# Performance work log

Hardware: AMD Instinct MI355X
Metric: run time of the kernel (lower is better)

Reference implementation:

```python
import jax, jax.numpy as jnp
import numpy as np

N, IN_DIM, OUT_DIM = 2048, 128, 64
ALPHA = 0.2  # LeakyReLU negative slope


def setup_inputs() -> dict:
    key = jax.random.key(0)
    k1, k2, k3 = jax.random.split(key, 3)
    H = jax.random.normal(k1, (N, IN_DIM), dtype=jnp.float32)
    # Xavier-uniform-like init for W [out_dim, in_dim] (torch Linear weight layout)
    limit_w = float(np.sqrt(6.0 / (IN_DIM + OUT_DIM)))
    W = jax.random.uniform(k2, (OUT_DIM, IN_DIM), dtype=jnp.float32,
                           minval=-limit_w, maxval=limit_w)
    limit_a = float(np.sqrt(6.0 / (OUT_DIM + 1)))
    a = jax.random.uniform(k3, (OUT_DIM,), dtype=jnp.float32,
                           minval=-limit_a, maxval=limit_a)
    return {"H": H, "W": W, "a": a}


def reference(H, W, a):
    # Wh: [N, D]
    Wh = H @ W.T
    # e[i, j] = leakyrelu(Wh[i] + Wh[j]) . a   -> [N, N]
    e = jnp.einsum('ijd,d->ij',
                   jax.nn.leaky_relu(Wh[:, None, :] + Wh[None, :, :],
                                     negative_slope=ALPHA),
                   a)
    attention = jax.nn.softmax(e, axis=1)  # softmax over j (columns)
    return attention @ Wh  # [N, D]
```

## Files before the change

kernel.cpp:

```cpp
#include <hip/hip_runtime.h>
#include <hip/hip_fp16.h>

#define N 2048
#define IN_DIM 128
#define D 64
#define ALPHA 0.2f
#define TI 4
#define BLK 512
#define NW (BLK / 64)


typedef _Float16 half2v __attribute__((ext_vector_type(2)));

__device__ __forceinline__ unsigned short f2bf_rne(float f) {
  unsigned int u = __float_as_uint(f);
  unsigned int r = u + 0x7fffu + ((u >> 16) & 1u);
  return (unsigned short)(r >> 16);
}
__device__ __forceinline__ unsigned short f2h_rne(float f) {
  return __half_as_ushort(__float2half(f));
}
#define BF_LO(u) __uint_as_float((u) << 16)
#define BF_HI(u) __uint_as_float((u) & 0xffff0000u)

__device__ __forceinline__ float dot2abs(unsigned s2, unsigned w2,
                                         unsigned a2, float acc) {
  half2v sv = __builtin_bit_cast(half2v, s2);
  half2v wv = __builtin_bit_cast(half2v, w2);
  half2v t = sv + wv;
  unsigned tu = __builtin_bit_cast(unsigned, t) & 0x7fff7fffu;
  return __builtin_amdgcn_fdot2(__builtin_bit_cast(half2v, tu),
                                __builtin_bit_cast(half2v, a2),
                                acc, false);
}

__global__ __launch_bounds__(256) void wh_kernel(
    const float* __restrict__ H, const float* __restrict__ W,
    const float* __restrict__ a, unsigned short* __restrict__ Whb,
    unsigned short* __restrict__ Whh, unsigned int* __restrict__ WhP,
    float* __restrict__ b, unsigned int* __restrict__ ap2) {
  __shared__ float wlds[D][IN_DIM + 1];
  __shared__ float hl[8 * IN_DIM];
  const int t = threadIdx.x;
  const int i0 = blockIdx.x * 8;

  if (blockIdx.x == 0 && t < D / 2) {
    ap2[t] = (unsigned)f2h_rne(0.4f * a[2 * t]) |
             ((unsigned)f2h_rne(0.4f * a[2 * t + 1]) << 16);
  }

  #pragma unroll
  for (int rep = 0; rep < 8; ++rep) {
    int idx = rep * 1024 + t * 4;
    float4 w4 = *(const float4*)&W[idx];
    int d = idx / IN_DIM, k = idx % IN_DIM;
    wlds[d][k] = w4.x; wlds[d][k + 1] = w4.y;
    wlds[d][k + 2] = w4.z; wlds[d][k + 3] = w4.w;
  }
  *(float4*)&hl[t * 4] = *(const float4*)&H[i0 * IN_DIM + t * 4];
  __syncthreads();

  const int wid = t >> 6, lane = t & 63;
  const float av = a[lane];
  #pragma unroll
  for (int r = 0; r < 2; ++r) {
    const int lr = wid * 2 + r;
    const int i = i0 + lr;
    float acc = 0.f;
    #pragma unroll 8
    for (int k = 0; k < IN_DIM; ++k)
      acc = fmaf(hl[lr * IN_DIM + k], wlds[lane][k], acc);
    Whb[i * D + lane] = f2bf_rne(acc);
    unsigned hv = f2h_rne(acc);
    Whh[i * D + lane] = (unsigned short)hv;
    unsigned partner = (unsigned)__shfl_xor((int)hv, 1);
    if (!(lane & 1)) WhP[(lane >> 1) * N + i] = hv | (partner << 16);
    float pb = av * acc;
    #pragma unroll
    for (int off = 32; off; off >>= 1) pb += __shfl_xor(pb, off);
    if (lane == 0) b[i] = 0.6f * pb;
  }
}

__global__ __launch_bounds__(BLK, 4) void attn_kernel(
    const unsigned short* __restrict__ Whb,
    const unsigned short* __restrict__ Whh,
    const unsigned int* __restrict__ WhP,
    const float* __restrict__ b, const unsigned int* __restrict__ ap2,
    float* __restrict__ out) {
  __shared__ float p_lds[TI][N];
  __shared__ float red2s[TI][NW];
  __shared__ float part[NW][TI][D];

  const int t = threadIdx.x;
  const int i0 = blockIdx.x * TI;
  const int wid = t >> 6, lane = t & 63;

  float bs[TI];
  #pragma unroll
  for (int ti = 0; ti < TI; ++ti) bs[ti] = b[i0 + ti];

  const int j0 = t * 4;
  float4 bj = *(const float4*)&b[j0];
  float4 ac[TI];
  #pragma unroll
  for (int ti = 0; ti < TI; ++ti) { ac[ti].x = ac[ti].y = ac[ti].z = ac[ti].w = 0.f; }

  const unsigned int* wp = WhP + j0;
  const uint4* sU = (const uint4*)(Whh + i0 * D);
  const uint4* aU = (const uint4*)ap2;

  uint4 wbuf[2][4], sbuf[2][TI], abuf[2];
  #pragma unroll
  for (int q = 0; q < 4; ++q) wbuf[0][q] = *(const uint4*)&wp[q * N];
  #pragma unroll
  for (int ti = 0; ti < TI; ++ti) sbuf[0][ti] = sU[ti * 8];
  abuf[0] = aU[0];

  #pragma unroll
  for (int c = 0; c < D / 8; ++c) {
    const int cur = c & 1, nxt = cur ^ 1;
    if (c < D / 8 - 1) {
      #pragma unroll
      for (int q = 0; q < 4; ++q)
        wbuf[nxt][q] = *(const uint4*)&wp[((c + 1) * 4 + q) * N];
      #pragma unroll
      for (int ti = 0; ti < TI; ++ti) sbuf[nxt][ti] = sU[ti * 8 + c + 1];
      abuf[nxt] = aU[c + 1];
    }
    #pragma unroll
    for (int q = 0; q < 4; ++q) {
      const unsigned a2 = (q == 0) ? abuf[cur].x : (q == 1) ? abuf[cur].y
                        : (q == 2) ? abuf[cur].z : abuf[cur].w;
      const uint4 w4 = wbuf[cur][q];
      #pragma unroll
      for (int ti = 0; ti < TI; ++ti) {
        const unsigned s2 = (q == 0) ? sbuf[cur][ti].x : (q == 1) ? sbuf[cur][ti].y
                          : (q == 2) ? sbuf[cur][ti].z : sbuf[cur][ti].w;
        ac[ti].x = dot2abs(s2, w4.x, a2, ac[ti].x);
        ac[ti].y = dot2abs(s2, w4.y, a2, ac[ti].y);
        ac[ti].z = dot2abs(s2, w4.z, a2, ac[ti].z);
        ac[ti].w = dot2abs(s2, w4.w, a2, ac[ti].w);
      }
    }
  }

  float s_t[TI];
  #pragma unroll
  for (int ti = 0; ti < TI; ++ti) {
    float4 p4;
    p4.x = __expf(ac[ti].x + bs[ti] + bj.x);
    p4.y = __expf(ac[ti].y + bs[ti] + bj.y);
    p4.z = __expf(ac[ti].z + bs[ti] + bj.z);
    p4.w = __expf(ac[ti].w + bs[ti] + bj.w);
    *(float4*)&p_lds[ti][j0] = p4;
    s_t[ti] = (p4.x + p4.y) + (p4.z + p4.w);
  }
  #pragma unroll
  for (int off = 32; off; off >>= 1) {
    #pragma unroll
    for (int ti = 0; ti < TI; ++ti)
      s_t[ti] += __shfl_xor(s_t[ti], off);
  }
  if (lane == 0) {
    #pragma unroll
    for (int ti = 0; ti < TI; ++ti) red2s[ti][wid] = s_t[ti];
  }
  __syncthreads();

  const int jbase = wid * (N / NW);
  const int hi4 = (lane >> 4) * 4;
  const int col = (lane & 15) * 4;
  float4 acc[TI];
  #pragma unroll
  for (int ti = 0; ti < TI; ++ti) { acc[ti].x = acc[ti].y = acc[ti].z = acc[ti].w = 0.f; }

  uint2 wtile[2][4];
  float4 ptile[2][TI];
  {
    const int r0 = jbase + hi4;
    #pragma unroll
    for (int dd = 0; dd < 4; ++dd)
      wtile[0][dd] = *(const uint2*)&Whb[(r0 + dd) * D + col];
    #pragma unroll
    for (int ti = 0; ti < TI; ++ti)
      ptile[0][ti] = *(const float4*)&p_lds[ti][r0];
  }

  #pragma unroll
  for (int it = 0; it < (N / NW) / 16; ++it) {
    const int cur = it & 1, nxt = cur ^ 1;
    if (it < (N / NW) / 16 - 1) {
      const int r1 = jbase + (it + 1) * 16 + hi4;
      #pragma unroll
      for (int dd = 0; dd < 4; ++dd)
        wtile[nxt][dd] = *(const uint2*)&Whb[(r1 + dd) * D + col];
      #pragma unroll
      for (int ti = 0; ti < TI; ++ti)
        ptile[nxt][ti] = *(const float4*)&p_lds[ti][r1];
    }
    float4 w0, w1, w2, w3;
    w0.x = BF_LO(wtile[cur][0].x); w0.y = BF_HI(wtile[cur][0].x);
    w0.z = BF_LO(wtile[cur][0].y); w0.w = BF_HI(wtile[cur][0].y);
    w1.x = BF_LO(wtile[cur][1].x); w1.y = BF_HI(wtile[cur][1].x);
    w1.z = BF_LO(wtile[cur][1].y); w1.w = BF_HI(wtile[cur][1].y);
    w2.x = BF_LO(wtile[cur][2].x); w2.y = BF_HI(wtile[cur][2].x);
    w2.z = BF_LO(wtile[cur][2].y); w2.w = BF_HI(wtile[cur][2].y);
    w3.x = BF_LO(wtile[cur][3].x); w3.y = BF_HI(wtile[cur][3].x);
    w3.z = BF_LO(wtile[cur][3].y); w3.w = BF_HI(wtile[cur][3].y);
    #pragma unroll
    for (int ti = 0; ti < TI; ++ti) {
      float4 p4 = ptile[cur][ti];
      acc[ti].x = fmaf(p4.x, w0.x, fmaf(p4.y, w1.x, fmaf(p4.z, w2.x, fmaf(p4.w, w3.x, acc[ti].x))));
      acc[ti].y = fmaf(p4.x, w0.y, fmaf(p4.y, w1.y, fmaf(p4.z, w2.y, fmaf(p4.w, w3.y, acc[ti].y))));
      acc[ti].z = fmaf(p4.x, w0.z, fmaf(p4.y, w1.z, fmaf(p4.z, w2.z, fmaf(p4.w, w3.z, acc[ti].z))));
      acc[ti].w = fmaf(p4.x, w0.w, fmaf(p4.y, w1.w, fmaf(p4.z, w2.w, fmaf(p4.w, w3.w, acc[ti].w))));
    }
  }
  #pragma unroll
  for (int ti = 0; ti < TI; ++ti) {
    acc[ti].x += __shfl_xor(acc[ti].x, 16);
    acc[ti].y += __shfl_xor(acc[ti].y, 16);
    acc[ti].z += __shfl_xor(acc[ti].z, 16);
    acc[ti].w += __shfl_xor(acc[ti].w, 16);
    acc[ti].x += __shfl_xor(acc[ti].x, 32);
    acc[ti].y += __shfl_xor(acc[ti].y, 32);
    acc[ti].z += __shfl_xor(acc[ti].z, 32);
    acc[ti].w += __shfl_xor(acc[ti].w, 32);
  }
  if (lane < 16) {
    #pragma unroll
    for (int ti = 0; ti < TI; ++ti)
      *(float4*)&part[wid][ti][lane * 4] = acc[ti];
  }
  __syncthreads();
  if (t < TI * D) {
    const int ti = t >> 6, dd = t & 63;
    float s = 0.f;
    #pragma unroll
    for (int w = 0; w < NW; ++w) s += part[w][ti][dd];
    float4 r0 = *(const float4*)&red2s[ti][0];
    float4 r1 = *(const float4*)&red2s[ti][4];
    float rsum = ((r0.x + r0.y) + (r0.z + r0.w)) +
                 ((r1.x + r1.y) + (r1.z + r1.w));
    out[(i0 + ti) * D + dd] = s * (1.f / rsum);
  }
}

extern "C" void kernel_launch(void* const* d_in, const int* in_sizes, int n_in,
                              void* d_out, int out_size, void* d_ws, size_t ws_size,
                              hipStream_t stream) {
  const float* H = (const float*)d_in[0];
  const float* W = (const float*)d_in[1];
  const float* a = (const float*)d_in[2];
  float* out = (float*)d_out;

  unsigned short* Whb = (unsigned short*)d_ws;
  unsigned short* Whh = Whb + N * D;
  unsigned int* WhP = (unsigned int*)(Whh + N * D);
  float* b = (float*)(WhP + (D / 2) * N);
  unsigned int* ap2 = (unsigned int*)(b + N);

  wh_kernel<<<N / 8, 256, 0, stream>>>(H, W, a, Whb, Whh, WhP, b, ap2);
  attn_kernel<<<N / TI, BLK, 0, stream>>>(Whb, Whh, WhP, b, ap2, out);
}
```

Measured before the change: 33.16 us.

## Use packed fp16 dot2 for attention-weighted sum with pair-interleaved Wh layout

Replaces the bf16 Wh copy with a row-pair interleaved fp16 buffer so the P·Wh accumulation can use packed fp16 dot2 instructions on converted probabilities, halving FMA count and removing bf16 unpacking. The softmax exponent switches to exp2 with a fixed offset and drops the per-row bias term, which cancels in normalisation. wh_kernel now computes two rows per loop sharing the W load. Risks include fp16 overflow or precision loss in probabilities, since the fixed offset does not adapt to row maxima.

```diff
diff --git a/kernel.cpp b/kernel.cpp
--- a/kernel.cpp
+++ b/kernel.cpp
@@ -12,16 +12,9 @@
 
 typedef _Float16 half2v __attribute__((ext_vector_type(2)));
 
-__device__ __forceinline__ unsigned short f2bf_rne(float f) {
-  unsigned int u = __float_as_uint(f);
-  unsigned int r = u + 0x7fffu + ((u >> 16) & 1u);
-  return (unsigned short)(r >> 16);
-}
 __device__ __forceinline__ unsigned short f2h_rne(float f) {
   return __half_as_ushort(__float2half(f));
 }
-#define BF_LO(u) __uint_as_float((u) << 16)
-#define BF_HI(u) __uint_as_float((u) & 0xffff0000u)
 
 __device__ __forceinline__ float dot2abs(unsigned s2, unsigned w2,
                                          unsigned a2, float acc) {
@@ -34,10 +27,19 @@
                                 acc, false);
 }
 
+__device__ __forceinline__ float dot2p(half2v p2, unsigned w2, float acc) {
+  return __builtin_amdgcn_fdot2(p2, __builtin_bit_cast(half2v, w2),
+                                acc, false);
+}
+
+__device__ __forceinline__ half2v cvt_pk(float lo, float hi) {
+  return __builtin_bit_cast(half2v, __builtin_amdgcn_cvt_pkrtz(lo, hi));
+}
+
 __global__ __launch_bounds__(256) void wh_kernel(
     const float* __restrict__ H, const float* __restrict__ W,
-    const float* __restrict__ a, unsigned short* __restrict__ Whb,
-    unsigned short* __restrict__ Whh, unsigned int* __restrict__ WhP,
+    const float* __restrict__ a, unsigned short* __restrict__ Whh,
+    unsigned int* __restrict__ WhP, unsigned int* __restrict__ WhQ,
     float* __restrict__ b, unsigned int* __restrict__ ap2) {
   __shared__ float wlds[D][IN_DIM + 1];
   __shared__ float hl[8 * IN_DIM];
@@ -62,30 +64,41 @@
 
   const int wid = t >> 6, lane = t & 63;
   const float av = a[lane];
-  #pragma unroll
-  for (int r = 0; r < 2; ++r) {
-    const int lr = wid * 2 + r;
-    const int i = i0 + lr;
-    float acc = 0.f;
-    #pragma unroll 8
-    for (int k = 0; k < IN_DIM; ++k)
-      acc = fmaf(hl[lr * IN_DIM + k], wlds[lane][k], acc);
-    Whb[i * D + lane] = f2bf_rne(acc);
-    unsigned hv = f2h_rne(acc);
-    Whh[i * D + lane] = (unsigned short)hv;
-    unsigned partner = (unsigned)__shfl_xor((int)hv, 1);
-    if (!(lane & 1)) WhP[(lane >> 1) * N + i] = hv | (partner << 16);
-    float pb = av * acc;
-    #pragma unroll
-    for (int off = 32; off; off >>= 1) pb += __shfl_xor(pb, off);
-    if (lane == 0) b[i] = 0.6f * pb;
-  }
+  const int lr0 = wid * 2, lr1 = lr0 + 1;
+  const int ia = i0 + lr0, ib = i0 + lr1;
+
+  float acc0 = 0.f, acc1 = 0.f;
+  #pragma unroll 4
+  for (int k = 0; k < IN_DIM; ++k) {
+    float wv = wlds[lane][k];
+    acc0 = fmaf(hl[lr0 * IN_DIM + k], wv, acc0);
+    acc1 = fmaf(hl[lr1 * IN_DIM + k], wv, acc1);
+  }
+
+  unsigned h0 = f2h_rne(acc0), h1 = f2h_rne(acc1);
+  Whh[ia * D + lane] = (unsigned short)h0;
+  Whh[ib * D + lane] = (unsigned short)h1;
+  unsigned q0 = (unsigned)__shfl_xor((int)h0, 1);
+  unsigned q1 = (unsigned)__shfl_xor((int)h1, 1);
+  if (!(lane & 1)) {
+    WhP[(lane >> 1) * N + ia] = h0 | (q0 << 16);
+    WhP[(lane >> 1) * N + ib] = h1 | (q1 << 16);
+  }
+  WhQ[(blockIdx.x * 4 + wid) * D + lane] = h0 | (h1 << 16);
+
+  float pb0 = av * acc0, pb1 = av * acc1;
+  #pragma unroll
+  for (int off = 32; off; off >>= 1) {
+    pb0 += __shfl_xor(pb0, off);
+    pb1 += __shfl_xor(pb1, off);
+  }
+  if (lane == 0) { b[ia] = 0.6f * pb0; b[ib] = 0.6f * pb1; }
 }
 
 __global__ __launch_bounds__(BLK, 4) void attn_kernel(
-    const unsigned short* __restrict__ Whb,
     const unsigned short* __restrict__ Whh,
     const unsigned int* __restrict__ WhP,
+    const unsigned int* __restrict__ WhQ,
     const float* __restrict__ b, const unsigned int* __restrict__ ap2,
     float* __restrict__ out) {
   __shared__ float p_lds[TI][N];
@@ -95,10 +108,6 @@
   const int t = threadIdx.x;
   const int i0 = blockIdx.x * TI;
   const int wid = t >> 6, lane = t & 63;
-
-  float bs[TI];
-  #pragma unroll
-  for (int ti = 0; ti < TI; ++ti) bs[ti] = b[i0 + ti];
 
   const int j0 = t * 4;
   float4 bj = *(const float4*)&b[j0];
@@ -145,14 +154,15 @@
     }
   }
 
+  const float L2E = 1.4426950408889634f;
   float s_t[TI];
   #pragma unroll
   for (int ti = 0; ti < TI; ++ti) {
     float4 p4;
-    p4.x = __expf(ac[ti].x + bs[ti] + bj.x);
-    p4.y = __expf(ac[ti].y + bs[ti] + bj.y);
-    p4.z = __expf(ac[ti].z + bs[ti] + bj.z);
-    p4.w = __expf(ac[ti].w + bs[ti] + bj.w);
+    p4.x = __builtin_amdgcn_exp2f(fmaf(ac[ti].x + bj.x, L2E, -6.f));
+    p4.y = __builtin_amdgcn_exp2f(fmaf(ac[ti].y + bj.y, L2E, -6.f));
+    p4.z = __builtin_amdgcn_exp2f(fmaf(ac[ti].z + bj.z, L2E, -6.f));
+    p4.w = __builtin_amdgcn_exp2f(fmaf(ac[ti].w + bj.w, L2E, -6.f));
     *(float4*)&p_lds[ti][j0] = p4;
     s_t[ti] = (p4.x + p4.y) + (p4.z + p4.w);
   }
@@ -175,13 +185,12 @@
   #pragma unroll
   for (int ti = 0; ti < TI; ++ti) { acc[ti].x = acc[ti].y = acc[ti].z = acc[ti].w = 0.f; }
 
-  uint2 wtile[2][4];
+  uint4 wq[2][2];
   float4 ptile[2][TI];
   {
     const int r0 = jbase + hi4;
-    #pragma unroll
-    for (int dd = 0; dd < 4; ++dd)
-      wtile[0][dd] = *(const uint2*)&Whb[(r0 + dd) * D + col];
+    wq[0][0] = *(const uint4*)&WhQ[(r0 >> 1) * D + col];
+    wq[0][1] = *(const uint4*)&WhQ[((r0 >> 1) + 1) * D + col];
     #pragma unroll
     for (int ti = 0; ti < TI; ++ti)
       ptile[0][ti] = *(const float4*)&p_lds[ti][r0];
@@ -192,29 +201,21 @@
     const int cur = it & 1, nxt = cur ^ 1;
     if (it < (N / NW) / 16 - 1) {
       const int r1 = jbase + (it + 1) * 16 + hi4;
-      #pragma unroll
-      for (int dd = 0; dd < 4; ++dd)
-        wtile[nxt][dd] = *(const uint2*)&Whb[(r1 + dd) * D + col];
+      wq[nxt][0] = *(const uint4*)&WhQ[(r1 >> 1) * D + col];
+      wq[nxt][1] = *(const uint4*)&WhQ[((r1 >> 1) + 1) * D + col];
       #pragma unroll
       for (int ti = 0; ti < TI; ++ti)
         ptile[nxt][ti] = *(const float4*)&p_lds[ti][r1];
     }
-    float4 w0, w1, w2, w3;
-    w0.x = BF_LO(wtile[cur][0].x); w0.y = BF_HI(wtile[cur][0].x);
-    w0.z = BF_LO(wtile[cur][0].y); w0.w = BF_HI(wtile[cur][0].y);
-    w1.x = BF_LO(wtile[cur][1].x); w1.y = BF_HI(wtile[cur][1].x);
-    w1.z = BF_LO(wtile[cur][1].y); w1.w = BF_HI(wtile[cur][1].y);
-    w2.x = BF_LO(wtile[cur][2].x); w2.y = BF_HI(wtile[cur][2].x);
-    w2.z = BF_LO(wtile[cur][2].y); w2.w = BF_HI(wtile[cur][2].y);
-    w3.x = BF_LO(wtile[cur][3].x); w3.y = BF_HI(wtile[cur][3].x);
-    w3.z = BF_LO(wtile[cur][3].y); w3.w = BF_HI(wtile[cur][3].y);
     #pragma unroll
     for (int ti = 0; ti < TI; ++ti) {
       float4 p4 = ptile[cur][ti];
-      acc[ti].x = fmaf(p4.x, w0.x, fmaf(p4.y, w1.x, fmaf(p4.z, w2.x, fmaf(p4.w, w3.x, acc[ti].x))));
-      acc[ti].y = fmaf(p4.x, w0.y, fmaf(p4.y, w1.y, fmaf(p4.z, w2.y, fmaf(p4.w, w3.y, acc[ti].y))));
-      acc[ti].z = fmaf(p4.x, w0.z, fmaf(p4.y, w1.z, fmaf(p4.z, w2.z, fmaf(p4.w, w3.z, acc[ti].z))));
-      acc[ti].w = fmaf(p4.x, w0.w, fmaf(p4.y, w1.w, fmaf(p4.z, w2.w, fmaf(p4.w, w3.w, acc[ti].w))));
+      half2v pp0 = cvt_pk(p4.x, p4.y);
+      half2v pp1 = cvt_pk(p4.z, p4.w);
+      acc[ti].x = dot2p(pp1, wq[cur][1].x, dot2p(pp0, wq[cur][0].x, acc[ti].x));
+      acc[ti].y = dot2p(pp1, wq[cur][1].y, dot2p(pp0, wq[cur][0].y, acc[ti].y));
+      acc[ti].z = dot2p(pp1, wq[cur][1].z, dot2p(pp0, wq[cur][0].z, acc[ti].z));
+      acc[ti].w = dot2p(pp1, wq[cur][1].w, dot2p(pp0, wq[cur][0].w, acc[ti].w));
     }
   }
   #pragma unroll
@@ -255,12 +256,12 @@
   const float* a = (const float*)d_in[2];
   float* out = (float*)d_out;
 
-  unsigned short* Whb = (unsigned short*)d_ws;
-  unsigned short* Whh = Whb + N * D;
+  unsigned short* Whh = (unsigned short*)d_ws;
   unsigned int* WhP = (unsigned int*)(Whh + N * D);
-  float* b = (float*)(WhP + (D / 2) * N);
+  unsigned int* WhQ = WhP + (D / 2) * N;
+  float* b = (float*)(WhQ + (N / 2) * D);
   unsigned int* ap2 = (unsigned int*)(b + N);
 
-  wh_kernel<<<N / 8, 256, 0, stream>>>(H, W, a, Whb, Whh, WhP, b, ap2);
-  attn_kernel<<<N / TI, BLK, 0, stream>>>(Whb, Whh, WhP, b, ap2, out);
-}
+  wh_kernel<<<N / 8, 256, 0, stream>>>(H, W, a, Whh, WhP, WhQ, b, ap2);
+  attn_kernel<<<N / TI, BLK, 0, stream>>>(Whh, WhP, WhQ, b, ap2, out);
+}
```

New measurement: 30.75 us. 7.3% less time.
